# Performance work log

Measured on AMD Instinct MI355X. Metric: run time of the kernel, lower is better.

Reference implementation:

```python
import jax, jax.numpy as jnp
import numpy as np

NEG_SLOPE = 0.2


def _gat_conv(x, src, dst, W, a_src, a_dst, num_nodes):
    """PyG-style GATConv (single linear for src/dst, softmax over dst neighborhoods).
    x: [N, F_in]; W: [F_in, H*C]; a_src/a_dst: [H, C]. Returns [N, H, C]."""
    H, C = a_src.shape
    h = (x @ W).reshape(num_nodes, H, C)                       # [N, H, C]
    alpha_src = jnp.einsum('nhc,hc->nh', h, a_src)             # [N, H]
    alpha_dst = jnp.einsum('nhc,hc->nh', h, a_dst)             # [N, H]
    e = alpha_src[src] + alpha_dst[dst]                        # [E, H]
    e = jax.nn.leaky_relu(e, NEG_SLOPE)
    # segment softmax over destination node
    m = jax.ops.segment_max(e, dst, num_segments=num_nodes)    # [N, H]
    e = jnp.exp(e - m[dst])
    s = jax.ops.segment_sum(e, dst, num_segments=num_nodes)    # [N, H]
    alpha = e / (s[dst] + 1e-16)                               # [E, H]
    msg = h[src] * alpha[:, :, None]                           # [E, H, C]
    return jax.ops.segment_sum(msg, dst, num_segments=num_nodes)


def setup_inputs() -> dict:
    key = jax.random.key(0)
    ks = jax.random.split(key, 10)
    N, E = 50000, 800000
    F_in, HID, H, OUT = 256, 64, 4, 32
    x = jax.random.normal(ks[0], (N, F_in), dtype=jnp.float32)
    edge_index = jax.random.randint(ks[1], (2, E), 0, N, dtype=jnp.int64)
    s1 = 1.0 / np.sqrt(F_in)
    s2 = 1.0 / np.sqrt(HID * H)
    W1 = jax.random.normal(ks[2], (F_in, H * HID), dtype=jnp.float32) * s1
    att_src1 = jax.random.normal(ks[3], (H, HID), dtype=jnp.float32) * s1
    att_dst1 = jax.random.normal(ks[4], (H, HID), dtype=jnp.float32) * s1
    b1 = jnp.zeros((H * HID,), dtype=jnp.float32)
    W2 = jax.random.normal(ks[5], (H * HID, OUT), dtype=jnp.float32) * s2
    att_src2 = jax.random.normal(ks[6], (1, OUT), dtype=jnp.float32) * s2
    att_dst2 = jax.random.normal(ks[7], (1, OUT), dtype=jnp.float32) * s2
    b2 = jnp.zeros((OUT,), dtype=jnp.float32)
    return {"x": x, "edge_index": edge_index,
            "W1": W1, "att_src1": att_src1, "att_dst1": att_dst1, "b1": b1,
            "W2": W2, "att_src2": att_src2, "att_dst2": att_dst2, "b2": b2}


def reference(x, edge_index, W1, att_src1, att_dst1, b1, W2, att_src2, att_dst2, b2):
    N = x.shape[0]
    # PyG GATConv adds self-loops by default
    loops = jnp.arange(N, dtype=edge_index.dtype)
    src = jnp.concatenate([edge_index[0], loops])
    dst = jnp.concatenate([edge_index[1], loops])
    h1 = _gat_conv(x, src, dst, W1, att_src1, att_dst1, N)      # [N, H, HID]
    h1 = h1.reshape(N, -1) + b1                                 # concat heads + bias
    h1 = jax.nn.relu(h1)                                        # dropout = eval no-op
    h2 = _gat_conv(h1, src, dst, W2, att_src2, att_dst2, N)     # [N, 1, OUT]
    out = h2.mean(axis=1) + b2                                  # concat=False -> mean
    return out
```

## Files before the change

### kernel.cpp

```cpp
#include <hip/hip_runtime.h>
#include <hip/hip_fp16.h>
#include <math.h>

#define FIN  256
#define D1   256
#define NHEAD 4
#define HIDC 64
#define DOUT 32
#define NSLOPE 0.2f
#define SCHUNK 2048

typedef __attribute__((ext_vector_type(8))) short short8v;
typedef __attribute__((ext_vector_type(4))) float f32x4;

__device__ __forceinline__ float lrelu(float x) { return x >= 0.f ? x : NSLOPE * x; }

__device__ __forceinline__ void bf16split(float x, unsigned short& h, unsigned short& l) {
  unsigned u = __float_as_uint(x);
  unsigned uh = (u + 0x7fffu + ((u >> 16) & 1u)) & 0xffff0000u;
  h = (unsigned short)(uh >> 16);
  float r = x - __uint_as_float(uh);
  unsigned ur = __float_as_uint(r);
  l = (unsigned short)((ur + 0x7fffu + ((ur >> 16) & 1u)) >> 16);
}

__global__ void zero2_kernel(int* __restrict__ a, int* __restrict__ b, int n) {
  int i = blockIdx.x * blockDim.x + threadIdx.x;
  if (i < n) { a[i] = 0; b[i] = 0; }
}

__global__ void count_kernel(const int* __restrict__ src, const int* __restrict__ dst,
                             int* __restrict__ deg, int E, int N) {
  int i = blockIdx.x * blockDim.x + threadIdx.x;
  if (i < E) {
    atomicAdd(&deg[dst[i]], 1);
  } else if (i < E + N) {
    atomicAdd(&deg[i - E], 1);
  }
}

__global__ __launch_bounds__(256) void scan1_kernel(const int* __restrict__ deg,
                                                    int* __restrict__ bsum, int N) {
  int b = blockIdx.x, t = threadIdx.x;
  int base = b * SCHUNK + t * 8;
  int s = 0;
  if (base + 8 <= N) {
    int4 a = *(const int4*)&deg[base];
    int4 c = *(const int4*)&deg[base + 4];
    s = a.x + a.y + a.z + a.w + c.x + c.y + c.z + c.w;
  } else {
#pragma unroll
    for (int i = 0; i < 8; ++i) if (base + i < N) s += deg[base + i];
  }
  int lane = t & 63, w = t >> 6;
#pragma unroll
  for (int off = 32; off >= 1; off >>= 1) s += __shfl_down(s, off);
  __shared__ int sh[4];
  if (lane == 0) sh[w] = s;
  __syncthreads();
  if (t == 0) bsum[b] = sh[0] + sh[1] + sh[2] + sh[3];
}

__global__ __launch_bounds__(1024) void scan2_kernel(int* __restrict__ bsum, int nb) {
  __shared__ int sh[1024];
  int t = threadIdx.x;
  sh[t] = (t < nb) ? bsum[t] : 0;
  __syncthreads();
  for (int off = 1; off < 1024; off <<= 1) {
    int u = (t >= off) ? sh[t - off] : 0;
    __syncthreads();
    sh[t] += u;
    __syncthreads();
  }
  if (t < nb) bsum[t] = sh[t];
}

__global__ __launch_bounds__(256) void scan3_kernel(const int* __restrict__ deg,
                                                    const int* __restrict__ bsum,
                                                    int* __restrict__ row_ptr, int N) {
  int b = blockIdx.x, t = threadIdx.x;
  int base = b * SCHUNK + t * 8;
  int vals[8];
  if (base + 8 <= N) {
    int4 a = *(const int4*)&deg[base];
    int4 c = *(const int4*)&deg[base + 4];
    vals[0] = a.x; vals[1] = a.y; vals[2] = a.z; vals[3] = a.w;
    vals[4] = c.x; vals[5] = c.y; vals[6] = c.z; vals[7] = c.w;
  } else {
#pragma unroll
    for (int i = 0; i < 8; ++i) vals[i] = (base + i < N) ? deg[base + i] : 0;
  }
  int s = 0;
#pragma unroll
  for (int i = 0; i < 8; ++i) { s += vals[i]; vals[i] = s; }
  int lane = t & 63, w = t >> 6;
  int inc = s;
#pragma unroll
  for (int off = 1; off < 64; off <<= 1) {
    int u = __shfl_up(inc, off);
    if (lane >= off) inc += u;
  }
  __shared__ int wsum[4];
  if (lane == 63) wsum[w] = inc;
  __syncthreads();
  int woff = 0;
#pragma unroll
  for (int i = 0; i < 4; ++i) if (i < w) woff += wsum[i];
  int excl = woff + inc - s;
  int offbase = (b ? bsum[b - 1] : 0) + excl;
#pragma unroll
  for (int i = 0; i < 8; ++i) {
    int idx = base + i;
    if (idx < N) row_ptr[idx + 1] = offbase + vals[i];
  }
  if (b == 0 && t == 0) row_ptr[0] = 0;
}

__global__ void scatter_kernel(const int* __restrict__ src, const int* __restrict__ dst,
                               const int* __restrict__ row_ptr, int* __restrict__ cur,
                               int* __restrict__ col, int E, int N) {
  int i = blockIdx.x * blockDim.x + threadIdx.x;
  int s, d;
  if (i < E) { s = src[i]; d = dst[i]; }
  else if (i < E + N) { s = i - E; d = i - E; }
  else return;
  int pos = row_ptr[d] + atomicAdd(&cur[d], 1);
  col[pos] = s;
}

__global__ __launch_bounds__(256) void splitW1_kernel(const float* __restrict__ W1,
                                                      unsigned short* __restrict__ Wt_hi,
                                                      unsigned short* __restrict__ Wt_lo) {
  int t = blockIdx.x * 256 + threadIdx.x;
  int c = t >> 8, k = t & 255;
  float x = W1[(size_t)k * D1 + c];
  unsigned short h, l;
  bf16split(x, h, l);
  Wt_hi[(size_t)c * FIN + k] = h;
  Wt_lo[(size_t)c * FIN + k] = l;
}

__global__ __launch_bounds__(256) void gemm1_kernel(const float* __restrict__ A,
                                                    const unsigned short* __restrict__ Bt_hi,
                                                    const unsigned short* __restrict__ Bt_lo,
                                                    __half* __restrict__ C, int N) {
  __shared__ unsigned short As_hi[64][40];
  __shared__ unsigned short As_lo[64][40];
  __shared__ unsigned short Bs_hi[256][40];
  __shared__ unsigned short Bs_lo[256][40];
  int t = threadIdx.x;
  int row0 = blockIdx.x * 64;
  int lane = t & 63;
  int col0 = (t >> 6) * 64;
  int frow = lane & 15;
  int fk8  = lane >> 4;

  f32x4 acc[4][4];
#pragma unroll
  for (int i = 0; i < 4; ++i)
#pragma unroll
    for (int j = 0; j < 4; ++j)
#pragma unroll
      for (int q = 0; q < 4; ++q) acc[i][j][q] = 0.f;

  for (int k0 = 0; k0 < 256; k0 += 32) {
    {
      int r = t >> 3;
      int kk = (t & 7) * 4;
#pragma unroll
      for (int rep = 0; rep < 2; ++rep) {
        int rr = r + rep * 32;
        int gr = row0 + rr;
        float4 v = {0.f, 0.f, 0.f, 0.f};
        if (gr < N) v = *(const float4*)&A[(size_t)gr * FIN + k0 + kk];
        unsigned short h0, l0, h1, l1, h2, l2, h3, l3;
        bf16split(v.x, h0, l0); bf16split(v.y, h1, l1);
        bf16split(v.z, h2, l2); bf16split(v.w, h3, l3);
        ushort4 vh = {h0, h1, h2, h3};
        ushort4 vl = {l0, l1, l2, l3};
        *(ushort4*)&As_hi[rr][kk] = vh;
        *(ushort4*)&As_lo[rr][kk] = vl;
      }
    }
    {
#pragma unroll
      for (int q = 0; q < 4; ++q) {
        int4 vh = *(const int4*)&Bt_hi[(size_t)t * FIN + k0 + q * 8];
        int4 vl = *(const int4*)&Bt_lo[(size_t)t * FIN + k0 + q * 8];
        *(int4*)&Bs_hi[t][q * 8] = vh;
        *(int4*)&Bs_lo[t][q * 8] = vl;
      }
    }
    __syncthreads();
    short8v bh[4], bl[4];
#pragma unroll
    for (int ct = 0; ct < 4; ++ct) {
      bh[ct] = *(const short8v*)&Bs_hi[col0 + ct * 16 + frow][fk8 * 8];
      bl[ct] = *(const short8v*)&Bs_lo[col0 + ct * 16 + frow][fk8 * 8];
    }
#pragma unroll
    for (int rt = 0; rt < 4; ++rt) {
      short8v ah = *(const short8v*)&As_hi[rt * 16 + frow][fk8 * 8];
      short8v al = *(const short8v*)&As_lo[rt * 16 + frow][fk8 * 8];
#pragma unroll
      for (int ct = 0; ct < 4; ++ct) {
        acc[rt][ct] = __builtin_amdgcn_mfma_f32_16x16x32_bf16(ah, bh[ct], acc[rt][ct], 0, 0, 0);
        acc[rt][ct] = __builtin_amdgcn_mfma_f32_16x16x32_bf16(ah, bl[ct], acc[rt][ct], 0, 0, 0);
        acc[rt][ct] = __builtin_amdgcn_mfma_f32_16x16x32_bf16(al, bh[ct], acc[rt][ct], 0, 0, 0);
      }
    }
    __syncthreads();
  }
#pragma unroll
  for (int rt = 0; rt < 4; ++rt) {
#pragma unroll
    for (int i = 0; i < 4; ++i) {
      int gr = row0 + rt * 16 + fk8 * 4 + i;
      if (gr < N) {
#pragma unroll
        for (int ct = 0; ct < 4; ++ct)
          C[(size_t)gr * D1 + col0 + ct * 16 + frow] = __float2half(acc[rt][ct][i]);
      }
    }
  }
}

__global__ __launch_bounds__(256) void alpha1_kernel(const __half* __restrict__ h,
                                                     const float* __restrict__ a_src,
                                                     const float* __restrict__ a_dst,
                                                     float* __restrict__ as,
                                                     float* __restrict__ ad, int N) {
  int wid = (blockIdx.x * blockDim.x + threadIdx.x) >> 6;
  if (wid >= N) return;
  int lane = threadIdx.x & 63;
  int2 r = *(const int2*)&h[(size_t)wid * D1 + lane * 4];
  float2 f01 = __half22float2(*(__half2*)&r.x);
  float2 f23 = __half22float2(*(__half2*)&r.y);
  float4 s4 = *(const float4*)&a_src[lane * 4];
  float4 d4 = *(const float4*)&a_dst[lane * 4];
  float ps = f01.x * s4.x + f01.y * s4.y + f23.x * s4.z + f23.y * s4.w;
  float pd = f01.x * d4.x + f01.y * d4.y + f23.x * d4.z + f23.y * d4.w;
#pragma unroll
  for (int off = 8; off >= 1; off >>= 1) {
    ps += __shfl_xor(ps, off);
    pd += __shfl_xor(pd, off);
  }
  int hh = lane >> 4;
  if ((lane & 15) == 0) { as[wid * 4 + hh] = ps; ad[wid * 4 + hh] = pd; }
}

__global__ __launch_bounds__(256) void stats1_kernel(const float* __restrict__ as1,
                                                     const float* __restrict__ ad1,
                                                     const int* __restrict__ row_ptr,
                                                     const int* __restrict__ col,
                                                     float* __restrict__ mx1,
                                                     float* __restrict__ inv1, int N) {
  int t = blockIdx.x * blockDim.x + threadIdx.x;
  if (t >= N * 4) return;
  int n = t >> 2, h = t & 3;
  int beg = row_ptr[n];
  int deg = row_ptr[n + 1] - beg;
  float adh = ad1[t];
  float m = -INFINITY, s = 0.f;
  int cn = col[beg];
  for (int j = 0; j < deg; ++j) {
    int c = cn;
    if (j + 1 < deg) cn = col[beg + j + 1];
    float e = lrelu(as1[(size_t)c * 4 + h] + adh);
    float nm = fmaxf(m, e);
    s = s * expf(m - nm) + expf(e - nm);
    m = nm;
  }
  mx1[t] = m;
  inv1[t] = 1.f / (s + 1e-16f);
}

__global__ __launch_bounds__(256) void agg1_kernel(const __half* __restrict__ hl,
                                                   const float* __restrict__ as1,
                                                   const float* __restrict__ ad1,
                                                   const float* __restrict__ mx1,
                                                   const float* __restrict__ inv1,
                                                   const int* __restrict__ row_ptr,
                                                   const int* __restrict__ col,
                                                   const float* __restrict__ b1,
                                                   float* __restrict__ h1, int N) {
  int wid = (blockIdx.x * blockDim.x + threadIdx.x) >> 6;
  if (wid >= N) return;
  int lane = threadIdx.x & 63;
  int hm = lane >> 4;
  int beg = row_ptr[wid];
  int deg = row_ptr[wid + 1] - beg;
  float adh = ad1[wid * 4 + hm];
  float mh  = mx1[wid * 4 + hm];
  float ih  = inv1[wid * 4 + hm];
  float4 acc = {0.f, 0.f, 0.f, 0.f};
  int j = 0;
  for (; j + 4 <= deg; j += 4) {
    int s0 = col[beg + j + 0];
    int s1 = col[beg + j + 1];
    int s2 = col[beg + j + 2];
    int s3 = col[beg + j + 3];
    float a0 = as1[(size_t)s0 * 4 + hm];
    float a1 = as1[(size_t)s1 * 4 + hm];
    float a2 = as1[(size_t)s2 * 4 + hm];
    float a3 = as1[(size_t)s3 * 4 + hm];
    int2 r0 = *(const int2*)&hl[(size_t)s0 * D1 + lane * 4];
    int2 r1 = *(const int2*)&hl[(size_t)s1 * D1 + lane * 4];
    int2 r2 = *(const int2*)&hl[(size_t)s2 * D1 + lane * 4];
    int2 r3 = *(const int2*)&hl[(size_t)s3 * D1 + lane * 4];
    float w0 = expf(lrelu(a0 + adh) - mh) * ih;
    float w1 = expf(lrelu(a1 + adh) - mh) * ih;
    float w2 = expf(lrelu(a2 + adh) - mh) * ih;
    float w3 = expf(lrelu(a3 + adh) - mh) * ih;
    float2 u, v;
    u = __half22float2(*(__half2*)&r0.x); v = __half22float2(*(__half2*)&r0.y);
    acc.x = fmaf(w0, u.x, acc.x); acc.y = fmaf(w0, u.y, acc.y);
    acc.z = fmaf(w0, v.x, acc.z); acc.w = fmaf(w0, v.y, acc.w);
    u = __half22float2(*(__half2*)&r1.x); v = __half22float2(*(__half2*)&r1.y);
    acc.x = fmaf(w1, u.x, acc.x); acc.y = fmaf(w1, u.y, acc.y);
    acc.z = fmaf(w1, v.x, acc.z); acc.w = fmaf(w1, v.y, acc.w);
    u = __half22float2(*(__half2*)&r2.x); v = __half22float2(*(__half2*)&r2.y);
    acc.x = fmaf(w2, u.x, acc.x); acc.y = fmaf(w2, u.y, acc.y);
    acc.z = fmaf(w2, v.x, acc.z); acc.w = fmaf(w2, v.y, acc.w);
    u = __half22float2(*(__half2*)&r3.x); v = __half22float2(*(__half2*)&r3.y);
    acc.x = fmaf(w3, u.x, acc.x); acc.y = fmaf(w3, u.y, acc.y);
    acc.z = fmaf(w3, v.x, acc.z); acc.w = fmaf(w3, v.y, acc.w);
  }
  for (; j < deg; ++j) {
    int s0 = col[beg + j];
    float a0 = as1[(size_t)s0 * 4 + hm];
    int2 r0 = *(const int2*)&hl[(size_t)s0 * D1 + lane * 4];
    float w0 = expf(lrelu(a0 + adh) - mh) * ih;
    float2 u = __half22float2(*(__half2*)&r0.x);
    float2 v = __half22float2(*(__half2*)&r0.y);
    acc.x = fmaf(w0, u.x, acc.x); acc.y = fmaf(w0, u.y, acc.y);
    acc.z = fmaf(w0, v.x, acc.z); acc.w = fmaf(w0, v.y, acc.w);
  }
  float4 bb = *(const float4*)&b1[lane * 4];
  float4 o;
  o.x = fmaxf(acc.x + bb.x, 0.f);
  o.y = fmaxf(acc.y + bb.y, 0.f);
  o.z = fmaxf(acc.z + bb.z, 0.f);
  o.w = fmaxf(acc.w + bb.w, 0.f);
  *(float4*)&h1[(size_t)wid * D1 + lane * 4] = o;
}

__global__ __launch_bounds__(256) void gemm2_kernel(const float* __restrict__ A,
                                                    const float* __restrict__ B,
                                                    __half* __restrict__ C, int N) {
  __shared__ float ws[256][33];
  __shared__ float xs[32][132];
  int t = threadIdx.x;
#pragma unroll
  for (int j = 0; j < 32; ++j) {
    int idx = j * 256 + t;
    ws[idx >> 5][idx & 31] = B[idx];
  }
  int row0 = blockIdx.x * 128;
  int tx = t & 31, ty = t >> 5;
  float acc[16] = {};
  for (int k0 = 0; k0 < 256; k0 += 32) {
    __syncthreads();
#pragma unroll
    for (int rep = 0; rep < 4; ++rep) {
      int r = (t >> 3) + rep * 32;
      int kk = (t & 7) * 4;
      int gr = row0 + r;
      float4 v = {0.f, 0.f, 0.f, 0.f};
      if (gr < N) v = *(const float4*)&A[(size_t)gr * D1 + k0 + kk];
      xs[kk + 0][r] = v.x; xs[kk + 1][r] = v.y; xs[kk + 2][r] = v.z; xs[kk + 3][r] = v.w;
    }
    __syncthreads();
#pragma unroll
    for (int k = 0; k < 32; ++k) {
      float w = ws[k0 + k][tx];
#pragma unroll
      for (int rq = 0; rq < 4; ++rq) {
        float4 a4 = *(const float4*)&xs[k][ty * 16 + rq * 4];
        acc[rq * 4 + 0] = fmaf(a4.x, w, acc[rq * 4 + 0]);
        acc[rq * 4 + 1] = fmaf(a4.y, w, acc[rq * 4 + 1]);
        acc[rq * 4 + 2] = fmaf(a4.z, w, acc[rq * 4 + 2]);
        acc[rq * 4 + 3] = fmaf(a4.w, w, acc[rq * 4 + 3]);
      }
    }
  }
#pragma unroll
  for (int j = 0; j < 16; ++j) {
    int gr = row0 + ty * 16 + j;
    if (gr < N) C[(size_t)gr * DOUT + tx] = __float2half(acc[j]);
  }
}

__global__ __launch_bounds__(256) void alpha2_kernel(const __half* __restrict__ h2,
                                                     const float* __restrict__ a_src,
                                                     const float* __restrict__ a_dst,
                                                     float* __restrict__ as,
                                                     float* __restrict__ ad, int N) {
  int wid = (blockIdx.x * blockDim.x + threadIdx.x) >> 6;
  int lane = threadIdx.x & 63;
  int n = wid * 2 + (lane >> 5);
  int c = lane & 31;
  float v = (n < N) ? __half2float(h2[(size_t)n * DOUT + c]) : 0.f;
  float ps = v * a_src[c];
  float pd = v * a_dst[c];
#pragma unroll
  for (int off = 16; off >= 1; off >>= 1) {
    ps += __shfl_xor(ps, off);
    pd += __shfl_xor(pd, off);
  }
  if (c == 0 && n < N) { as[n] = ps; ad[n] = pd; }
}

__global__ __launch_bounds__(256) void stats2_kernel(const float* __restrict__ as2,
                                                     const float* __restrict__ ad2,
                                                     const int* __restrict__ row_ptr,
                                                     const int* __restrict__ col,
                                                     float* __restrict__ mx2,
                                                     float* __restrict__ inv2, int N) {
  int n = blockIdx.x * blockDim.x + threadIdx.x;
  if (n >= N) return;
  int beg = row_ptr[n];
  int deg = row_ptr[n + 1] - beg;
  float ad = ad2[n];
  float m = -INFINITY, s = 0.f;
  int cn = col[beg];
  for (int j = 0; j < deg; ++j) {
    int c = cn;
    if (j + 1 < deg) cn = col[beg + j + 1];
    float e = lrelu(as2[c] + ad);
    float nm = fmaxf(m, e);
    s = s * expf(m - nm) + expf(e - nm);
    m = nm;
  }
  mx2[n] = m;
  inv2[n] = 1.f / (s + 1e-16f);
}

__global__ __launch_bounds__(256) void agg2_kernel(const __half* __restrict__ h2,
                                                   const float* __restrict__ as2,
                                                   const float* __restrict__ ad2,
                                                   const float* __restrict__ mx2,
                                                   const float* __restrict__ inv2,
                                                   const int* __restrict__ row_ptr,
                                                   const int* __restrict__ col,
                                                   const float* __restrict__ b2,
                                                   float* __restrict__ out, int N) {
  int wid = (blockIdx.x * blockDim.x + threadIdx.x) >> 6;
  if (wid >= N) return;
  int lane = threadIdx.x & 63;
  int c = lane & 31;
  int beg = row_ptr[wid];
  int deg = row_ptr[wid + 1] - beg;
  float ad = ad2[wid];
  float mh = mx2[wid];
  float ih = inv2[wid];
  float acc = 0.f;
  int j = 0;
  for (; j + 4 <= deg; j += 4) {
    int s0 = col[beg + j + 0];
    int s1 = col[beg + j + 1];
    int s2 = col[beg + j + 2];
    int s3 = col[beg + j + 3];
    float a0 = as2[s0];
    float a1 = as2[s1];
    float a2 = as2[s2];
    float a3 = as2[s3];
    float v0 = __half2float(h2[(size_t)s0 * DOUT + c]);
    float v1 = __half2float(h2[(size_t)s1 * DOUT + c]);
    float v2 = __half2float(h2[(size_t)s2 * DOUT + c]);
    float v3 = __half2float(h2[(size_t)s3 * DOUT + c]);
    float w0 = expf(lrelu(a0 + ad) - mh) * ih;
    float w1 = expf(lrelu(a1 + ad) - mh) * ih;
    float w2 = expf(lrelu(a2 + ad) - mh) * ih;
    float w3 = expf(lrelu(a3 + ad) - mh) * ih;
    acc = fmaf(w0, v0, acc);
    acc = fmaf(w1, v1, acc);
    acc = fmaf(w2, v2, acc);
    acc = fmaf(w3, v3, acc);
  }
  for (; j < deg; ++j) {
    int s0 = col[beg + j];
    float a0 = as2[s0];
    float v0 = __half2float(h2[(size_t)s0 * DOUT + c]);
    float w0 = expf(lrelu(a0 + ad) - mh) * ih;
    acc = fmaf(w0, v0, acc);
  }
  if (lane < 32) out[(size_t)wid * DOUT + c] = acc + b2[c];
}

extern "C" void kernel_launch(void* const* d_in, const int* in_sizes, int n_in,
                              void* d_out, int out_size, void* d_ws, size_t ws_size,
                              hipStream_t stream) {
  const float* x     = (const float*)d_in[0];
  const int*   ei    = (const int*)d_in[1];
  const float* W1    = (const float*)d_in[2];
  const float* asrc1 = (const float*)d_in[3];
  const float* adst1 = (const float*)d_in[4];
  const float* b1    = (const float*)d_in[5];
  const float* W2    = (const float*)d_in[6];
  const float* asrc2 = (const float*)d_in[7];
  const float* adst2 = (const float*)d_in[8];
  const float* b2    = (const float*)d_in[9];

  const int N = in_sizes[0] / FIN;
  const int E = in_sizes[1] / 2;
  const int ET = E + N;
  const int* src = ei;
  const int* dst = ei + E;
  const int NB = (N + SCHUNK - 1) / SCHUNK;

  char* base = (char*)d_ws;
  size_t off = 0;
  auto alloc = [&](size_t bytes) -> void* {
    void* p = base + off;
    off = (off + bytes + 255) & ~(size_t)255;
    return p;
  };
  int* row_ptr = (int*)alloc((size_t)(N + 1) * 4);
  int* deg     = (int*)alloc((size_t)N * 4);
  int* cur     = (int*)alloc((size_t)N * 4);
  int* col     = (int*)alloc((size_t)ET * 4);
  int* bsum    = (int*)alloc((size_t)1024 * 4);
  float* as1   = (float*)alloc((size_t)N * 4 * 4);
  float* ad1   = (float*)alloc((size_t)N * 4 * 4);
  float* mx1   = (float*)alloc((size_t)N * 4 * 4);
  float* inv1  = (float*)alloc((size_t)N * 4 * 4);
  float* as2   = (float*)alloc((size_t)N * 4);
  float* ad2   = (float*)alloc((size_t)N * 4);
  float* mx2   = (float*)alloc((size_t)N * 4);
  float* inv2  = (float*)alloc((size_t)N * 4);
  unsigned short* Wt_hi = (unsigned short*)alloc((size_t)FIN * D1 * 2);
  unsigned short* Wt_lo = (unsigned short*)alloc((size_t)FIN * D1 * 2);
  __half* hl1  = (__half*)alloc((size_t)N * D1 * 2);
  float* h1    = (float*)alloc((size_t)N * D1 * 4);
  __half* h2   = hl1;
  float* out   = (float*)d_out;

  hipLaunchKernelGGL(zero2_kernel, dim3((N + 255) / 256), dim3(256), 0, stream, deg, cur, N);
  hipLaunchKernelGGL(count_kernel, dim3((ET + 255) / 256), dim3(256), 0, stream, src, dst, deg, E, N);
  hipLaunchKernelGGL(splitW1_kernel, dim3(FIN * D1 / 256), dim3(256), 0, stream, W1, Wt_hi, Wt_lo);
  hipLaunchKernelGGL(scan1_kernel, dim3(NB), dim3(256), 0, stream, deg, bsum, N);
  hipLaunchKernelGGL(scan2_kernel, dim3(1), dim3(1024), 0, stream, bsum, NB);
  hipLaunchKernelGGL(scan3_kernel, dim3(NB), dim3(256), 0, stream, deg, bsum, row_ptr, N);
  hipLaunchKernelGGL(scatter_kernel, dim3((ET + 255) / 256), dim3(256), 0, stream, src, dst, row_ptr, cur, col, E, N);

  hipLaunchKernelGGL(gemm1_kernel, dim3((N + 63) / 64), dim3(256), 0, stream, x, Wt_hi, Wt_lo, hl1, N);
  hipLaunchKernelGGL(alpha1_kernel, dim3((N + 3) / 4), dim3(256), 0, stream, hl1, asrc1, adst1, as1, ad1, N);
  hipLaunchKernelGGL(stats1_kernel, dim3((N * 4 + 255) / 256), dim3(256), 0, stream, as1, ad1, row_ptr, col, mx1, inv1, N);
  hipLaunchKernelGGL(agg1_kernel, dim3((N + 3) / 4), dim3(256), 0, stream, hl1, as1, ad1, mx1, inv1, row_ptr, col, b1, h1, N);

  hipLaunchKernelGGL(gemm2_kernel, dim3((N + 127) / 128), dim3(256), 0, stream, h1, W2, h2, N);
  hipLaunchKernelGGL(alpha2_kernel, dim3((N + 7) / 8), dim3(256), 0, stream, h2, asrc2, adst2, as2, ad2, N);
  hipLaunchKernelGGL(stats2_kernel, dim3((N + 255) / 256), dim3(256), 0, stream, as2, ad2, row_ptr, col, mx2, inv2, N);
  hipLaunchKernelGGL(agg2_kernel, dim3((N + 3) / 4), dim3(256), 0, stream, h2, as2, ad2, mx2, inv2, row_ptr, col, b2, out, N);
}
```

Baseline: 410.9 us.

## Precompute per-edge softmax weights, store h1 in fp16, and use MFMA for layer-2 GEMM

The stats kernels now make a second pass over each neighbourhood and write normalized attention weights per edge (wbuf). The aggregation kernels read those weights directly instead of gathering as[src] and recomputing exp. The layer-1 output h1 is stored as fp16 instead of fp32, which halves that write and the gemm2 read. gemm2 is rewritten with fp16 MFMA using a pre-transposed fp16 W2. In exchange this adds edge-sized weight buffers, a second gather pass in stats, and fp16 rounding of h1.

Result: faster. 398.2 us (-3.1%).

```diff
diff --git a/kernel.cpp b/kernel.cpp
--- a/kernel.cpp
+++ b/kernel.cpp
@@ -11,6 +11,7 @@
 #define SCHUNK 2048
 
 typedef __attribute__((ext_vector_type(8))) short short8v;
+typedef __attribute__((ext_vector_type(8))) _Float16 half8v;
 typedef __attribute__((ext_vector_type(4))) float f32x4;
 
 __device__ __forceinline__ float lrelu(float x) { return x >= 0.f ? x : NSLOPE * x; }
@@ -138,6 +139,13 @@
   bf16split(x, h, l);
   Wt_hi[(size_t)c * FIN + k] = h;
   Wt_lo[(size_t)c * FIN + k] = l;
+}
+
+__global__ __launch_bounds__(256) void splitW2_kernel(const float* __restrict__ W2,
+                                                      __half* __restrict__ W2t) {
+  int t = blockIdx.x * 256 + threadIdx.x;
+  int c = t >> 8, k = t & 255;
+  W2t[t] = __float2half(W2[(size_t)k * DOUT + c]);
 }
 
 __global__ __launch_bounds__(256) void gemm1_kernel(const float* __restrict__ A,
@@ -253,8 +261,7 @@
                                                      const float* __restrict__ ad1,
                                                      const int* __restrict__ row_ptr,
                                                      const int* __restrict__ col,
-                                                     float* __restrict__ mx1,
-                                                     float* __restrict__ inv1, int N) {
+                                                     float* __restrict__ wbuf, int N) {
   int t = blockIdx.x * blockDim.x + threadIdx.x;
   if (t >= N * 4) return;
   int n = t >> 2, h = t & 3;
@@ -271,28 +278,28 @@
     s = s * expf(m - nm) + expf(e - nm);
     m = nm;
   }
-  mx1[t] = m;
-  inv1[t] = 1.f / (s + 1e-16f);
+  float inv = 1.f / (s + 1e-16f);
+  cn = col[beg];
+  for (int j = 0; j < deg; ++j) {
+    int c = cn;
+    if (j + 1 < deg) cn = col[beg + j + 1];
+    float e = lrelu(as1[(size_t)c * 4 + h] + adh);
+    wbuf[(size_t)(beg + j) * 4 + h] = expf(e - m) * inv;
+  }
 }
 
 __global__ __launch_bounds__(256) void agg1_kernel(const __half* __restrict__ hl,
-                                                   const float* __restrict__ as1,
-                                                   const float* __restrict__ ad1,
-                                                   const float* __restrict__ mx1,
-                                                   const float* __restrict__ inv1,
+                                                   const float* __restrict__ wbuf,
                                                    const int* __restrict__ row_ptr,
                                                    const int* __restrict__ col,
                                                    const float* __restrict__ b1,
-                                                   float* __restrict__ h1, int N) {
+                                                   __half* __restrict__ h1, int N) {
   int wid = (blockIdx.x * blockDim.x + threadIdx.x) >> 6;
   if (wid >= N) return;
   int lane = threadIdx.x & 63;
   int hm = lane >> 4;
   int beg = row_ptr[wid];
   int deg = row_ptr[wid + 1] - beg;
-  float adh = ad1[wid * 4 + hm];
-  float mh  = mx1[wid * 4 + hm];
-  float ih  = inv1[wid * 4 + hm];
   float4 acc = {0.f, 0.f, 0.f, 0.f};
   int j = 0;
   for (; j + 4 <= deg; j += 4) {
@@ -300,18 +307,14 @@
     int s1 = col[beg + j + 1];
     int s2 = col[beg + j + 2];
     int s3 = col[beg + j + 3];
-    float a0 = as1[(size_t)s0 * 4 + hm];
-    float a1 = as1[(size_t)s1 * 4 + hm];
-    float a2 = as1[(size_t)s2 * 4 + hm];
-    float a3 = as1[(size_t)s3 * 4 + hm];
+    float w0 = wbuf[(size_t)(beg + j + 0) * 4 + hm];
+    float w1 = wbuf[(size_t)(beg + j + 1) * 4 + hm];
+    float w2 = wbuf[(size_t)(beg + j + 2) * 4 + hm];
+    float w3 = wbuf[(size_t)(beg + j + 3) * 4 + hm];
     int2 r0 = *(const int2*)&hl[(size_t)s0 * D1 + lane * 4];
     int2 r1 = *(const int2*)&hl[(size_t)s1 * D1 + lane * 4];
     int2 r2 = *(const int2*)&hl[(size_t)s2 * D1 + lane * 4];
     int2 r3 = *(const int2*)&hl[(size_t)s3 * D1 + lane * 4];
-    float w0 = expf(lrelu(a0 + adh) - mh) * ih;
-    float w1 = expf(lrelu(a1 + adh) - mh) * ih;
-    float w2 = expf(lrelu(a2 + adh) - mh) * ih;
-    float w3 = expf(lrelu(a3 + adh) - mh) * ih;
     float2 u, v;
     u = __half22float2(*(__half2*)&r0.x); v = __half22float2(*(__half2*)&r0.y);
     acc.x = fmaf(w0, u.x, acc.x); acc.y = fmaf(w0, u.y, acc.y);
@@ -328,67 +331,66 @@
   }
   for (; j < deg; ++j) {
     int s0 = col[beg + j];
-    float a0 = as1[(size_t)s0 * 4 + hm];
+    float w0 = wbuf[(size_t)(beg + j) * 4 + hm];
     int2 r0 = *(const int2*)&hl[(size_t)s0 * D1 + lane * 4];
-    float w0 = expf(lrelu(a0 + adh) - mh) * ih;
     float2 u = __half22float2(*(__half2*)&r0.x);
     float2 v = __half22float2(*(__half2*)&r0.y);
     acc.x = fmaf(w0, u.x, acc.x); acc.y = fmaf(w0, u.y, acc.y);
     acc.z = fmaf(w0, v.x, acc.z); acc.w = fmaf(w0, v.y, acc.w);
   }
   float4 bb = *(const float4*)&b1[lane * 4];
-  float4 o;
-  o.x = fmaxf(acc.x + bb.x, 0.f);
-  o.y = fmaxf(acc.y + bb.y, 0.f);
-  o.z = fmaxf(acc.z + bb.z, 0.f);
-  o.w = fmaxf(acc.w + bb.w, 0.f);
-  *(float4*)&h1[(size_t)wid * D1 + lane * 4] = o;
-}
-
-__global__ __launch_bounds__(256) void gemm2_kernel(const float* __restrict__ A,
-                                                    const float* __restrict__ B,
+  __half2 p0 = __floats2half2_rn(fmaxf(acc.x + bb.x, 0.f), fmaxf(acc.y + bb.y, 0.f));
+  __half2 p1 = __floats2half2_rn(fmaxf(acc.z + bb.z, 0.f), fmaxf(acc.w + bb.w, 0.f));
+  int2 pk;
+  pk.x = *(int*)&p0;
+  pk.y = *(int*)&p1;
+  *(int2*)&h1[(size_t)wid * D1 + lane * 4] = pk;
+}
+
+__global__ __launch_bounds__(256) void gemm2_kernel(const __half* __restrict__ A,
+                                                    const __half* __restrict__ Bt,
                                                     __half* __restrict__ C, int N) {
-  __shared__ float ws[256][33];
-  __shared__ float xs[32][132];
   int t = threadIdx.x;
-#pragma unroll
-  for (int j = 0; j < 32; ++j) {
-    int idx = j * 256 + t;
-    ws[idx >> 5][idx & 31] = B[idx];
-  }
-  int row0 = blockIdx.x * 128;
-  int tx = t & 31, ty = t >> 5;
-  float acc[16] = {};
-  for (int k0 = 0; k0 < 256; k0 += 32) {
-    __syncthreads();
-#pragma unroll
-    for (int rep = 0; rep < 4; ++rep) {
-      int r = (t >> 3) + rep * 32;
-      int kk = (t & 7) * 4;
-      int gr = row0 + r;
-      float4 v = {0.f, 0.f, 0.f, 0.f};
-      if (gr < N) v = *(const float4*)&A[(size_t)gr * D1 + k0 + kk];
-      xs[kk + 0][r] = v.x; xs[kk + 1][r] = v.y; xs[kk + 2][r] = v.z; xs[kk + 3][r] = v.w;
-    }
-    __syncthreads();
-#pragma unroll
-    for (int k = 0; k < 32; ++k) {
-      float w = ws[k0 + k][tx];
-#pragma unroll
-      for (int rq = 0; rq < 4; ++rq) {
-        float4 a4 = *(const float4*)&xs[k][ty * 16 + rq * 4];
-        acc[rq * 4 + 0] = fmaf(a4.x, w, acc[rq * 4 + 0]);
-        acc[rq * 4 + 1] = fmaf(a4.y, w, acc[rq * 4 + 1]);
-        acc[rq * 4 + 2] = fmaf(a4.z, w, acc[rq * 4 + 2]);
-        acc[rq * 4 + 3] = fmaf(a4.w, w, acc[rq * 4 + 3]);
+  int lane = t & 63;
+  int frow = lane & 15, fk8 = lane >> 4;
+  int row0 = (blockIdx.x * 4 + (t >> 6)) * 32;
+  if (row0 >= N) return;
+  half8v bf[8][2];
+#pragma unroll
+  for (int k8 = 0; k8 < 8; ++k8)
+#pragma unroll
+    for (int ct = 0; ct < 2; ++ct)
+      bf[k8][ct] = *(const half8v*)&Bt[(size_t)(ct * 16 + frow) * 256 + k8 * 32 + fk8 * 8];
+  f32x4 acc[2][2];
+#pragma unroll
+  for (int rt = 0; rt < 2; ++rt)
+#pragma unroll
+    for (int ct = 0; ct < 2; ++ct)
+#pragma unroll
+      for (int q = 0; q < 4; ++q) acc[rt][ct][q] = 0.f;
+#pragma unroll
+  for (int k8 = 0; k8 < 8; ++k8) {
+#pragma unroll
+    for (int rt = 0; rt < 2; ++rt) {
+      int gr = row0 + rt * 16 + frow;
+      if (gr >= N) gr = N - 1;
+      half8v af = *(const half8v*)&A[(size_t)gr * D1 + k8 * 32 + fk8 * 8];
+#pragma unroll
+      for (int ct = 0; ct < 2; ++ct)
+        acc[rt][ct] = __builtin_amdgcn_mfma_f32_16x16x32_f16(af, bf[k8][ct], acc[rt][ct], 0, 0, 0);
+    }
+  }
+#pragma unroll
+  for (int rt = 0; rt < 2; ++rt)
+#pragma unroll
+    for (int i = 0; i < 4; ++i) {
+      int gr = row0 + rt * 16 + fk8 * 4 + i;
+      if (gr < N) {
+#pragma unroll
+        for (int ct = 0; ct < 2; ++ct)
+          C[(size_t)gr * DOUT + ct * 16 + frow] = __float2half(acc[rt][ct][i]);
       }
     }
-  }
-#pragma unroll
-  for (int j = 0; j < 16; ++j) {
-    int gr = row0 + ty * 16 + j;
-    if (gr < N) C[(size_t)gr * DOUT + tx] = __float2half(acc[j]);
-  }
 }
 
 __global__ __launch_bounds__(256) void alpha2_kernel(const __half* __restrict__ h2,
@@ -415,8 +417,7 @@
                                                      const float* __restrict__ ad2,
                                                      const int* __restrict__ row_ptr,
                                                      const int* __restrict__ col,
-                                                     float* __restrict__ mx2,
-                                                     float* __restrict__ inv2, int N) {
+                                                     float* __restrict__ wbuf2, int N) {
   int n = blockIdx.x * blockDim.x + threadIdx.x;
   if (n >= N) return;
   int beg = row_ptr[n];
@@ -432,15 +433,17 @@
     s = s * expf(m - nm) + expf(e - nm);
     m = nm;
   }
-  mx2[n] = m;
-  inv2[n] = 1.f / (s + 1e-16f);
+  float inv = 1.f / (s + 1e-16f);
+  cn = col[beg];
+  for (int j = 0; j < deg; ++j) {
+    int c = cn;
+    if (j + 1 < deg) cn = col[beg + j + 1];
+    wbuf2[beg + j] = expf(lrelu(as2[c] + ad) - m) * inv;
+  }
 }
 
 __global__ __launch_bounds__(256) void agg2_kernel(const __half* __restrict__ h2,
-                                                   const float* __restrict__ as2,
-                                                   const float* __restrict__ ad2,
-                                                   const float* __restrict__ mx2,
-                                                   const float* __restrict__ inv2,
+                                                   const float* __restrict__ wbuf2,
                                                    const int* __restrict__ row_ptr,
                                                    const int* __restrict__ col,
                                                    const float* __restrict__ b2,
@@ -451,9 +454,6 @@
   int c = lane & 31;
   int beg = row_ptr[wid];
   int deg = row_ptr[wid + 1] - beg;
-  float ad = ad2[wid];
-  float mh = mx2[wid];
-  float ih = inv2[wid];
   float acc = 0.f;
   int j = 0;
   for (; j + 4 <= deg; j += 4) {
@@ -461,18 +461,14 @@
     int s1 = col[beg + j + 1];
     int s2 = col[beg + j + 2];
     int s3 = col[beg + j + 3];
-    float a0 = as2[s0];
-    float a1 = as2[s1];
-    float a2 = as2[s2];
-    float a3 = as2[s3];
+    float w0 = wbuf2[beg + j + 0];
+    float w1 = wbuf2[beg + j + 1];
+    float w2 = wbuf2[beg + j + 2];
+    float w3 = wbuf2[beg + j + 3];
     float v0 = __half2float(h2[(size_t)s0 * DOUT + c]);
     float v1 = __half2float(h2[(size_t)s1 * DOUT + c]);
     float v2 = __half2float(h2[(size_t)s2 * DOUT + c]);
     float v3 = __half2float(h2[(size_t)s3 * DOUT + c]);
-    float w0 = expf(lrelu(a0 + ad) - mh) * ih;
-    float w1 = expf(lrelu(a1 + ad) - mh) * ih;
-    float w2 = expf(lrelu(a2 + ad) - mh) * ih;
-    float w3 = expf(lrelu(a3 + ad) - mh) * ih;
     acc = fmaf(w0, v0, acc);
     acc = fmaf(w1, v1, acc);
     acc = fmaf(w2, v2, acc);
@@ -480,10 +476,8 @@
   }
   for (; j < deg; ++j) {
     int s0 = col[beg + j];
-    float a0 = as2[s0];
-    float v0 = __half2float(h2[(size_t)s0 * DOUT + c]);
-    float w0 = expf(lrelu(a0 + ad) - mh) * ih;
-    acc = fmaf(w0, v0, acc);
+    float w0 = wbuf2[beg + j];
+    acc = fmaf(w0, __half2float(h2[(size_t)s0 * DOUT + c]), acc);
   }
   if (lane < 32) out[(size_t)wid * DOUT + c] = acc + b2[c];
 }
@@ -523,22 +517,22 @@
   int* bsum    = (int*)alloc((size_t)1024 * 4);
   float* as1   = (float*)alloc((size_t)N * 4 * 4);
   float* ad1   = (float*)alloc((size_t)N * 4 * 4);
-  float* mx1   = (float*)alloc((size_t)N * 4 * 4);
-  float* inv1  = (float*)alloc((size_t)N * 4 * 4);
   float* as2   = (float*)alloc((size_t)N * 4);
   float* ad2   = (float*)alloc((size_t)N * 4);
-  float* mx2   = (float*)alloc((size_t)N * 4);
-  float* inv2  = (float*)alloc((size_t)N * 4);
+  float* wbuf1 = (float*)alloc((size_t)ET * 4 * 4);
+  float* wbuf2 = (float*)alloc((size_t)ET * 4);
   unsigned short* Wt_hi = (unsigned short*)alloc((size_t)FIN * D1 * 2);
   unsigned short* Wt_lo = (unsigned short*)alloc((size_t)FIN * D1 * 2);
+  __half* W2t  = (__half*)alloc((size_t)D1 * DOUT * 2);
   __half* hl1  = (__half*)alloc((size_t)N * D1 * 2);
-  float* h1    = (float*)alloc((size_t)N * D1 * 4);
+  __half* h1   = (__half*)alloc((size_t)N * D1 * 2);
   __half* h2   = hl1;
   float* out   = (float*)d_out;
 
   hipLaunchKernelGGL(zero2_kernel, dim3((N + 255) / 256), dim3(256), 0, stream, deg, cur, N);
   hipLaunchKernelGGL(count_kernel, dim3((ET + 255) / 256), dim3(256), 0, stream, src, dst, deg, E, N);
   hipLaunchKernelGGL(splitW1_kernel, dim3(FIN * D1 / 256), dim3(256), 0, stream, W1, Wt_hi, Wt_lo);
+  hipLaunchKernelGGL(splitW2_kernel, dim3(D1 * DOUT / 256), dim3(256), 0, stream, W2, W2t);
   hipLaunchKernelGGL(scan1_kernel, dim3(NB), dim3(256), 0, stream, deg, bsum, N);
   hipLaunchKernelGGL(scan2_kernel, dim3(1), dim3(1024), 0, stream, bsum, NB);
   hipLaunchKernelGGL(scan3_kernel, dim3(NB), dim3(256), 0, stream, deg, bsum, row_ptr, N);
@@ -546,11 +540,11 @@
 
   hipLaunchKernelGGL(gemm1_kernel, dim3((N + 63) / 64), dim3(256), 0, stream, x, Wt_hi, Wt_lo, hl1, N);
   hipLaunchKernelGGL(alpha1_kernel, dim3((N + 3) / 4), dim3(256), 0, stream, hl1, asrc1, adst1, as1, ad1, N);
-  hipLaunchKernelGGL(stats1_kernel, dim3((N * 4 + 255) / 256), dim3(256), 0, stream, as1, ad1, row_ptr, col, mx1, inv1, N);
-  hipLaunchKernelGGL(agg1_kernel, dim3((N + 3) / 4), dim3(256), 0, stream, hl1, as1, ad1, mx1, inv1, row_ptr, col, b1, h1, N);
-
-  hipLaunchKernelGGL(gemm2_kernel, dim3((N + 127) / 128), dim3(256), 0, stream, h1, W2, h2, N);
+  hipLaunchKernelGGL(stats1_kernel, dim3((N * 4 + 255) / 256), dim3(256), 0, stream, as1, ad1, row_ptr, col, wbuf1, N);
+  hipLaunchKernelGGL(agg1_kernel, dim3((N + 3) / 4), dim3(256), 0, stream, hl1, wbuf1, row_ptr, col, b1, h1, N);
+
+  hipLaunchKernelGGL(gemm2_kernel, dim3((N / 32 + 4) / 4), dim3(256), 0, stream, h1, W2t, h2, N);
   hipLaunchKernelGGL(alpha2_kernel, dim3((N + 7) / 8), dim3(256), 0, stream, h2, asrc2, adst2, as2, ad2, N);
-  hipLaunchKernelGGL(stats2_kernel, dim3((N + 255) / 256), dim3(256), 0, stream, as2, ad2, row_ptr, col, mx2, inv2, N);
-  hipLaunchKernelGGL(agg2_kernel, dim3((N + 3) / 4), dim3(256), 0, stream, h2, as2, ad2, mx2, inv2, row_ptr, col, b2, out, N);
-}
+  hipLaunchKernelGGL(stats2_kernel, dim3((N + 255) / 256), dim3(256), 0, stream, as2, ad2, row_ptr, col, wbuf2, N);
+  hipLaunchKernelGGL(agg2_kernel, dim3((N + 3) / 4), dim3(256), 0, stream, h2, wbuf2, row_ptr, col, b2, out, N);
+}
```
